# Optimization experiments

Hardware: AMD Instinct MI355X
Metric: run time of the kernel (lower is better)

The kernel has to match this reference:

```python
import jax, jax.numpy as jnp
import numpy as np

DIM = 768
D_STATE = 16
D_INNER = 2 * DIM  # expand=2


def setup_inputs() -> dict:
    key = jax.random.key(0)
    k_x, k_in, k_conv, k_out = jax.random.split(key, 4)
    B, L = 1, 4096
    x = jax.random.normal(k_x, (B, L, DIM), dtype=jnp.float32)
    # torch Linear weight layout: [out_features, in_features]
    W_in = jax.random.normal(k_in, (3 * D_INNER + 2 * D_STATE, DIM), dtype=jnp.float32) * 0.02
    # depthwise conv1d kernel: [out_ch=d_inner, in_ch/groups=1, k=3]
    W_conv = jax.random.normal(k_conv, (D_INNER, 1, 3), dtype=jnp.float32) * 0.1
    W_out = jax.random.normal(k_out, (DIM, D_INNER), dtype=jnp.float32) * 0.02
    A_log = jnp.log(jnp.tile(jnp.arange(1, D_STATE + 1, dtype=jnp.float32), (D_INNER, 1)))
    D = jnp.ones((D_INNER,), dtype=jnp.float32)
    return {"x": x, "W_in": W_in, "W_conv": W_conv, "W_out": W_out, "A_log": A_log, "D": D}


def reference(x, W_in, W_conv, W_out, A_log, D):
    d_inner = W_conv.shape[0]
    d_state = A_log.shape[1]
    Bsz = x.shape[0]

    xz = x @ W_in.T  # [B, L, 3*d_inner + 2*d_state]
    x_inner, z, B_ssm, C_ssm, delta = jnp.split(
        xz, [d_inner, 2 * d_inner, 2 * d_inner + d_state, 2 * d_inner + 2 * d_state], axis=-1
    )

    # depthwise conv over sequence: [B, d_inner, L]
    xc = jax.lax.conv_general_dilated(
        x_inner.transpose(0, 2, 1), W_conv,
        window_strides=(1,), padding=[(1, 1)], feature_group_count=d_inner,
    ).transpose(0, 2, 1)  # back to [B, L, d_inner]
    xc = jax.nn.silu(xc)

    A = -jnp.exp(A_log)  # [d_inner, d_state]
    delta = jax.nn.softplus(delta)  # [B, L, d_inner]
    dA = jnp.exp(jnp.einsum('bld,dn->bldn', delta, A))           # [B, L, d_inner, d_state]
    dBx = jnp.einsum('bld,bln,bld->bldn', delta, B_ssm, xc)      # delta_B * x fused

    def step(h, inp):
        da_t, dbx_t, c_t = inp  # [B,d,n], [B,d,n], [B,n]
        h = da_t * h + dbx_t
        y_t = jnp.einsum('bdn,bn->bd', h, c_t)
        return h, y_t

    h0 = jnp.zeros((Bsz, d_inner, d_state), dtype=x.dtype)
    _, ys = jax.lax.scan(
        step, h0,
        (dA.transpose(1, 0, 2, 3), dBx.transpose(1, 0, 2, 3), C_ssm.transpose(1, 0, 2)),
    )  # ys: [L, B, d_inner]

    y = ys.transpose(1, 0, 2) + xc * D  # skip connection
    y = y * jax.nn.silu(z)
    return y @ W_out.T  # [B, L, dim]
```

## Files before the change

kernel.cpp:

```cpp
#include <hip/hip_runtime.h>
#include <hip/hip_bf16.h>
#include <math.h>

#define LSEQ   4096
#define DIM    768
#define DINNER 1536
#define DSTATE 16
#define NCOLS  4640
#define NCH    256
#define CLEN   16
#define NPAD   4736
#define DXW    1568

typedef _Float16 f16;
typedef __attribute__((ext_vector_type(2))) _Float16 f16x2;
typedef __attribute__((ext_vector_type(4))) _Float16 f16x4;
typedef __attribute__((ext_vector_type(8))) _Float16 f16x8;
typedef __attribute__((ext_vector_type(4))) float f32x4;

__device__ __forceinline__ void gld_lds16(void* lds_dst, const void* gsrc) {
    __builtin_amdgcn_global_load_lds(
        (__attribute__((address_space(1))) void*)(gsrc),
        (__attribute__((address_space(3))) void*)(lds_dst), 16, 0, 0);
}

#define G1K    768
#define G1_NT  12
#define G1_BM  256
#define G1_BN  128
#define G1_RT  384
#define G1_LDSE (G1_RT * 64)

__global__ __launch_bounds__(512) void gemm1_pipe(const f16* __restrict__ A,
                                                  const f16* __restrict__ B,
                                                  float* __restrict__ C,
                                                  f16* __restrict__ Xb,
                                                  f16* __restrict__ Zb) {
    __shared__ __align__(16) f16 S[3 * G1_LDSE];

    const int P   = gridDim.x >> 3;
    const int idx = (blockIdx.x & 7) * P + (blockIdx.x >> 3);
    const int sm  = idx / 296;
    const int rem = idx - sm * 296;
    const int m0  = (sm * 8 + (rem & 7)) * G1_BM;
    const int n0  = (rem >> 3) * G1_BN;

    const int tid  = threadIdx.x;
    const int w    = tid >> 6;
    const int lane = tid & 63;
    const int wr   = w >> 1;
    const int wc   = w & 1;
    const int m    = lane & 15;
    const int q    = lane >> 4;
    const int rl8  = lane >> 3;
    const int bsel = lane & 7;

    const f16* gb[6];
#pragma unroll
    for (int s = 0; s < 6; ++s) {
        const int rl  = (w + 8 * s) * 8 + rl8;
        const int blk = bsel ^ (rl & 7);
        gb[s] = (rl < G1_BM) ? A + (size_t)(m0 + rl) * G1K + blk * 8
                             : B + (size_t)(n0 + rl - G1_BM) * G1K + blk * 8;
    }

    f32x4 acc[4][4];
#pragma unroll
    for (int i = 0; i < 4; i++)
#pragma unroll
        for (int j = 0; j < 4; j++) acc[i][j] = (f32x4){0.f, 0.f, 0.f, 0.f};

    auto stg2 = [&](int kt, int s0) {
        f16* dst = S + (kt % 3) * G1_LDSE;
#pragma unroll
        for (int s = s0; s < s0 + 2; ++s)
            gld_lds16(dst + (w + 8 * s) * 512, gb[s] + kt * 64);
    };
    auto stg6 = [&](int kt) {
        f16* dst = S + (kt % 3) * G1_LDSE;
#pragma unroll
        for (int s = 0; s < 6; ++s)
            gld_lds16(dst + (w + 8 * s) * 512, gb[s] + kt * 64);
    };

    stg6(0);
    stg6(1);

#pragma unroll
    for (int kt = 0; kt < G1_NT; ++kt) {
        if (kt < G1_NT - 1) asm volatile("s_waitcnt vmcnt(6)" ::: "memory");
        else                asm volatile("s_waitcnt vmcnt(0)" ::: "memory");
        __builtin_amdgcn_s_barrier();
        const f16* As = S + (kt % 3) * G1_LDSE;
        const f16* Bs = As + G1_BM * 64;
        const bool pf = (kt + 2 < G1_NT);

        f16x8 af0[2][2], af2[2][2], bh0[2][2], bh2[2][2];

#pragma unroll
        for (int kk = 0; kk < 2; ++kk) {
            const int fo = (((q + 4 * kk) ^ (m & 7)) << 3);
#pragma unroll
            for (int i = 0; i < 2; ++i) {
                af0[kk][i] = *(const f16x8*)&As[(wr * 64 + i * 16 + m) * 64 + fo];
                bh0[kk][i] = *(const f16x8*)&Bs[(wc * 64 + i * 16 + m) * 64 + fo];
            }
        }
        if (pf) stg2(kt + 2, 0);
        __builtin_amdgcn_s_barrier();
        asm volatile("s_waitcnt lgkmcnt(0)" ::: "memory");
        __builtin_amdgcn_sched_barrier(0);
        __builtin_amdgcn_s_setprio(1);
#pragma unroll
        for (int kk = 0; kk < 2; ++kk)
#pragma unroll
            for (int i = 0; i < 2; ++i)
#pragma unroll
                for (int j = 0; j < 2; ++j)
                    acc[i][j] = __builtin_amdgcn_mfma_f32_16x16x32_f16(
                        af0[kk][i], bh0[kk][j], acc[i][j], 0, 0, 0);
        __builtin_amdgcn_s_setprio(0);

#pragma unroll
        for (int kk = 0; kk < 2; ++kk) {
            const int fo = (((q + 4 * kk) ^ (m & 7)) << 3);
#pragma unroll
            for (int j = 0; j < 2; ++j)
                bh2[kk][j] = *(const f16x8*)&Bs[(wc * 64 + (j + 2) * 16 + m) * 64 + fo];
        }
        if (pf) stg2(kt + 2, 2);
        __builtin_amdgcn_s_barrier();
        asm volatile("s_waitcnt lgkmcnt(0)" ::: "memory");
        __builtin_amdgcn_sched_barrier(0);
        __builtin_amdgcn_s_setprio(1);
#pragma unroll
        for (int kk = 0; kk < 2; ++kk)
#pragma unroll
            for (int i = 0; i < 2; ++i)
#pragma unroll
                for (int j = 0; j < 2; ++j)
                    acc[i][j + 2] = __builtin_amdgcn_mfma_f32_16x16x32_f16(
                        af0[kk][i], bh2[kk][j], acc[i][j + 2], 0, 0, 0);
        __builtin_amdgcn_s_setprio(0);

#pragma unroll
        for (int kk = 0; kk < 2; ++kk) {
            const int fo = (((q + 4 * kk) ^ (m & 7)) << 3);
#pragma unroll
            for (int i = 0; i < 2; ++i)
                af2[kk][i] = *(const f16x8*)&As[(wr * 64 + (i + 2) * 16 + m) * 64 + fo];
        }
        if (pf) stg2(kt + 2, 4);
        __builtin_amdgcn_s_barrier();
        asm volatile("s_waitcnt lgkmcnt(0)" ::: "memory");
        __builtin_amdgcn_sched_barrier(0);
        __builtin_amdgcn_s_setprio(1);
#pragma unroll
        for (int kk = 0; kk < 2; ++kk)
#pragma unroll
            for (int i = 0; i < 2; ++i)
#pragma unroll
                for (int j = 0; j < 2; ++j)
                    acc[i + 2][j] = __builtin_amdgcn_mfma_f32_16x16x32_f16(
                        af2[kk][i], bh0[kk][j], acc[i + 2][j], 0, 0, 0);
        __builtin_amdgcn_s_setprio(0);

        __builtin_amdgcn_s_setprio(1);
#pragma unroll
        for (int kk = 0; kk < 2; ++kk)
#pragma unroll
            for (int i = 0; i < 2; ++i)
#pragma unroll
                for (int j = 0; j < 2; ++j)
                    acc[i + 2][j + 2] = __builtin_amdgcn_mfma_f32_16x16x32_f16(
                        af2[kk][i], bh2[kk][j], acc[i + 2][j + 2], 0, 0, 0);
        __builtin_amdgcn_s_setprio(0);
    }

    if (n0 < DINNER) {
#pragma unroll
        for (int i = 0; i < 4; i++)
#pragma unroll
            for (int j = 0; j < 4; j++) {
                const int col  = n0 + wc * 64 + j * 16 + m;
                const int rowb = m0 + wr * 64 + i * 16 + q * 4;
#pragma unroll
                for (int r = 0; r < 4; r++)
                    Xb[(size_t)(rowb + r) * DINNER + col] = (f16)acc[i][j][r];
            }
        return;
    }
    if (n0 < 2 * DINNER) {
#pragma unroll
        for (int i = 0; i < 4; i++)
#pragma unroll
            for (int j = 0; j < 4; j++) {
                const int col  = n0 - DINNER + wc * 64 + j * 16 + m;
                const int rowb = m0 + wr * 64 + i * 16 + q * 4;
#pragma unroll
                for (int r = 0; r < 4; r++)
                    Zb[(size_t)(rowb + r) * DINNER + col] = (f16)acc[i][j][r];
            }
        return;
    }
#pragma unroll
    for (int i = 0; i < 4; i++)
#pragma unroll
        for (int j = 0; j < 4; j++) {
            const int col = n0 - 2 * DINNER + wc * 64 + j * 16 + m;
            if (col >= DXW) continue;
            const int rowb = m0 + wr * 64 + i * 16 + q * 4;
#pragma unroll
            for (int r = 0; r < 4; r++)
                C[(size_t)(rowb + r) * DXW + col] = acc[i][j][r];
        }
}

#define G2K    1536
#define G2_NT  24
#define G2_LDSE (128 * 64)

__global__ __launch_bounds__(256) void gemm2_pipe(const f16* __restrict__ A,
                                                  const f16* __restrict__ B,
                                                  float* __restrict__ C) {
    __shared__ __align__(16) f16 S[3 * G2_LDSE];

    const int P   = gridDim.x >> 3;
    const int idx = (blockIdx.x & 7) * P + (blockIdx.x >> 3);
    const int m0  = (idx / 12) * 64;
    const int n0  = (idx % 12) * 64;

    const int tid  = threadIdx.x;
    const int w    = tid >> 6;
    const int lane = tid & 63;
    const int wr   = w >> 1;
    const int wc   = w & 1;
    const int m    = lane & 15;
    const int q    = lane >> 4;
    const int rl8  = lane >> 3;
    const int bsel = lane & 7;

    const f16* gb[4];
#pragma unroll
    for (int s = 0; s < 4; ++s) {
        const int rl  = (w + 4 * s) * 8 + rl8;
        const int blk = bsel ^ (rl & 7);
        gb[s] = (rl < 64) ? A + (size_t)(m0 + rl) * G2K + blk * 8
                          : B + (size_t)(n0 + rl - 64) * G2K + blk * 8;
    }

    f32x4 acc[2][2];
#pragma unroll
    for (int i = 0; i < 2; i++)
#pragma unroll
        for (int j = 0; j < 2; j++) acc[i][j] = (f32x4){0.f, 0.f, 0.f, 0.f};

    auto stg = [&](int kt) {
        f16* dst = S + (kt % 3) * G2_LDSE;
#pragma unroll
        for (int s = 0; s < 4; ++s)
            gld_lds16(dst + (w + 4 * s) * 512, gb[s] + kt * 64);
    };

    stg(0);
    stg(1);

#pragma unroll
    for (int kt = 0; kt < G2_NT; ++kt) {
        if (kt < G2_NT - 1) asm volatile("s_waitcnt vmcnt(4)" ::: "memory");
        else                asm volatile("s_waitcnt vmcnt(0)" ::: "memory");
        __builtin_amdgcn_s_barrier();
        if (kt + 2 < G2_NT) stg(kt + 2);

        const f16* As = S + (kt % 3) * G2_LDSE;
        const f16* Bs = As + 64 * 64;

        f16x8 af[2][2], bh[2][2];
#pragma unroll
        for (int kk = 0; kk < 2; ++kk) {
            const int fo = (((q + 4 * kk) ^ (m & 7)) << 3);
#pragma unroll
            for (int i = 0; i < 2; ++i) {
                af[kk][i] = *(const f16x8*)&As[(wr * 32 + i * 16 + m) * 64 + fo];
                bh[kk][i] = *(const f16x8*)&Bs[(wc * 32 + i * 16 + m) * 64 + fo];
            }
        }
        asm volatile("s_waitcnt lgkmcnt(0)" ::: "memory");
        __builtin_amdgcn_sched_barrier(0);
        __builtin_amdgcn_s_setprio(1);
#pragma unroll
        for (int kk = 0; kk < 2; ++kk)
#pragma unroll
            for (int i = 0; i < 2; ++i)
#pragma unroll
                for (int j = 0; j < 2; ++j)
                    acc[i][j] = __builtin_amdgcn_mfma_f32_16x16x32_f16(
                        af[kk][i], bh[kk][j], acc[i][j], 0, 0, 0);
        __builtin_amdgcn_s_setprio(0);
    }

#pragma unroll
    for (int i = 0; i < 2; i++)
#pragma unroll
        for (int j = 0; j < 2; j++) {
            const int col  = n0 + wc * 32 + j * 16 + m;
            const int rowb = m0 + wr * 32 + i * 16 + q * 4;
#pragma unroll
            for (int r = 0; r < 4; r++)
                C[(size_t)(rowb + r) * DIM + col] = acc[i][j][r];
        }
}

#define E0 (LSEQ * DIM)
#define E1 (E0 + NPAD * DIM)
#define E2 (E1 + DIM * DINNER)

__global__ __launch_bounds__(256) void cvt_all(const float* __restrict__ x,
                                               const float* __restrict__ Wi,
                                               const float* __restrict__ Wo,
                                               f16* __restrict__ Ax,
                                               f16* __restrict__ Bw,
                                               f16* __restrict__ Bo) {
    int i = (blockIdx.x * 256 + threadIdx.x) * 4;
    if (i < E0) {
        float4 v = *(const float4*)(x + i);
        f16x4 o = {(f16)v.x, (f16)v.y, (f16)v.z, (f16)v.w};
        *(f16x4*)(Ax + i) = o;
    } else if (i < E1) {
        int e = i - E0;
        int n = e / DIM;
        if (n < NCOLS) {
            float4 v = *(const float4*)(Wi + e);
            f16x4 o = {(f16)v.x, (f16)v.y, (f16)v.z, (f16)v.w};
            *(f16x4*)(Bw + e) = o;
        } else {
            f16x4 o = {(f16)0.f, (f16)0.f, (f16)0.f, (f16)0.f};
            *(f16x4*)(Bw + e) = o;
        }
    } else if (i < E2) {
        int e = i - E1;
        float4 v = *(const float4*)(Wo + e);
        f16x4 o = {(f16)v.x, (f16)v.y, (f16)v.z, (f16)v.w};
        *(f16x4*)(Bo + e) = o;
    }
}

__global__ __launch_bounds__(256, 3) void scan1_kernel(const float* __restrict__ Dxz,
                                                       const f16* __restrict__ Xb,
                                                       const float* __restrict__ Wc,
                                                       const float* __restrict__ A_log,
                                                       float* __restrict__ Sb,
                                                       float* __restrict__ hend) {
    __shared__ __align__(16) f16   Xs[18 * 512];
    __shared__ __align__(16) float Ds[16 * 512];
    __shared__ float Bs[CLEN * DSTATE];
    const int tid  = threadIdx.x;
    const int w4   = tid >> 6;
    const int lane = tid & 63;
    const int ch0  = blockIdx.x * 512;
    const int d0   = ch0 + 2 * tid;
    const int c    = blockIdx.y;
    const int l0   = c * CLEN;

    for (int r = w4; r < 18; r += 4) {
        const int gr = l0 - 1 + r;
        if (gr >= 0 && gr < LSEQ)
            gld_lds16(Xs + r * 512, Xb + (size_t)gr * DINNER + ch0 + lane * 8);
    }
    for (int i = w4; i < 32; i += 4) {
        const int t = i >> 1, hh = i & 1;
        gld_lds16(Ds + t * 512 + hh * 256,
                  Dxz + (size_t)(l0 + t) * DXW + 32 + ch0 + hh * 256 + lane * 4);
    }
    for (int i = tid; i < CLEN * DSTATE; i += 256)
        Bs[i] = Dxz[(size_t)(l0 + (i >> 4)) * DXW + (i & 15)];

    float Ar0[DSTATE], Ar1[DSTATE];
#pragma unroll
    for (int n = 0; n < DSTATE; n++) {
        Ar0[n] = -__expf(A_log[d0 * DSTATE + n]);
        Ar1[n] = -__expf(A_log[(d0 + 1) * DSTATE + n]);
    }
    const float w00 = Wc[d0 * 3 + 0], w01 = Wc[d0 * 3 + 1], w02 = Wc[d0 * 3 + 2];
    const float w10 = Wc[d0 * 3 + 3], w11 = Wc[d0 * 3 + 4], w12 = Wc[d0 * 3 + 5];

    asm volatile("s_waitcnt vmcnt(0)" ::: "memory");
    if (l0 == 0)
        *(f16x2*)&Xs[2 * tid] = (f16x2){(f16)0.f, (f16)0.f};
    if (c == NCH - 1)
        *(f16x2*)&Xs[17 * 512 + 2 * tid] = (f16x2){(f16)0.f, (f16)0.f};
    __syncthreads();

    auto ldx = [&](int r) -> float2 {
        f16x2 v = *(const f16x2*)&Xs[r * 512 + 2 * tid];
        return make_float2((float)v.x, (float)v.y);
    };

    float h0[DSTATE], h1[DSTATE];
#pragma unroll
    for (int n = 0; n < DSTATE; n++) { h0[n] = 0.f; h1[n] = 0.f; }
    float S0 = 0.f, S1 = 0.f;

    float2 xm = ldx(0);
    float2 x0 = ldx(1);
    for (int t = 0; t < CLEN; t++) {
        float2 xp = ldx(t + 2);
        float2 dr = *(const float2*)&Ds[t * 512 + 2 * tid];
        float v0  = xm.x * w00 + x0.x * w01 + xp.x * w02;
        float v1  = xm.y * w10 + x0.y * w11 + xp.y * w12;
        float xc0 = __fdividef(v0, 1.f + __expf(-v0));
        float xc1 = __fdividef(v1, 1.f + __expf(-v1));
        float dt0 = (dr.x > 20.f) ? dr.x : __logf(1.f + __expf(dr.x));
        float dt1 = (dr.y > 20.f) ? dr.y : __logf(1.f + __expf(dr.y));
        float u0 = dt0 * xc0, u1 = dt1 * xc1;
        S0 += dt0; S1 += dt1;
#pragma unroll
        for (int n = 0; n < DSTATE; n++) {
            float b = Bs[t * DSTATE + n];
            h0[n] = __expf(dt0 * Ar0[n]) * h0[n] + u0 * b;
            h1[n] = __expf(dt1 * Ar1[n]) * h1[n] + u1 * b;
        }
        xm = x0; x0 = xp;
    }
    *(float2*)&Sb[(size_t)c * DINNER + d0] = make_float2(S0, S1);
#pragma unroll
    for (int n = 0; n < DSTATE; n++)
        *(float2*)&hend[((size_t)c * DSTATE + n) * DINNER + d0] = make_float2(h0[n], h1[n]);
}

__global__ __launch_bounds__(256) void scan2_kernel(const float* __restrict__ Sb,
                                                    const float* __restrict__ A_log,
                                                    const float* __restrict__ hend,
                                                    float* __restrict__ hinit) {
    __shared__ float As_[16][17];
    __shared__ float Es_[16][17];
    __shared__ float Hs_[16][17];
    const int tid = threadIdx.x;
    const int el  = tid & 15;
    const int grp = tid >> 4;
    const int g   = blockIdx.x * 16 + el;
    const int n   = g / DINNER;
    const int d   = g - n * DINNER;
    const float Ar = -__expf(A_log[d * DSTATE + n]);
    const size_t S = (size_t)DSTATE * DINNER;

    float sv[16], ev[16];
#pragma unroll
    for (int k = 0; k < 16; ++k) {
        const int c = grp * 16 + k;
        sv[k] = Sb[(size_t)c * DINNER + d];
        ev[k] = hend[(size_t)c * S + g];
    }
    float av[16];
    float A = 1.f, E = 0.f;
#pragma unroll
    for (int k = 0; k < 16; ++k) {
        av[k] = __expf(sv[k] * Ar);
        E = av[k] * E + ev[k];
        A = av[k] * A;
    }
    As_[grp][el] = A;
    Es_[grp][el] = E;
    __syncthreads();
    if (tid < 16) {
        float h = 0.f;
#pragma unroll
        for (int gq = 0; gq < 16; ++gq) {
            Hs_[gq][tid] = h;
            h = As_[gq][tid] * h + Es_[gq][tid];
        }
    }
    __syncthreads();
    float h = Hs_[grp][el];
#pragma unroll
    for (int k = 0; k < 16; ++k) {
        const int c = grp * 16 + k;
        hinit[(size_t)c * S + g] = h;
        h = av[k] * h + ev[k];
    }
}

__global__ __launch_bounds__(256, 3) void scan3_kernel(const float* __restrict__ Dxz,
                                                       const f16* __restrict__ Xb,
                                                       const f16* __restrict__ Zb,
                                                       const float* __restrict__ Wc,
                                                       const float* __restrict__ A_log,
                                                       const float* __restrict__ hinit,
                                                       const float* __restrict__ Dp,
                                                       f16* __restrict__ Ay) {
    __shared__ __align__(16) f16   Xs[18 * 512];
    __shared__ __align__(16) float Ds[16 * 512];
    __shared__ float Bs[CLEN * DSTATE];
    __shared__ float Cs[CLEN * DSTATE];
    const int tid  = threadIdx.x;
    const int w4   = tid >> 6;
    const int lane = tid & 63;
    const int ch0  = blockIdx.x * 512;
    const int d0   = ch0 + 2 * tid;
    const int c    = blockIdx.y;
    const int l0   = c * CLEN;

    for (int r = w4; r < 18; r += 4) {
        const int gr = l0 - 1 + r;
        if (gr >= 0 && gr < LSEQ)
            gld_lds16(Xs + r * 512, Xb + (size_t)gr * DINNER + ch0 + lane * 8);
    }
    for (int i = w4; i < 32; i += 4) {
        const int t = i >> 1, hh = i & 1;
        gld_lds16(Ds + t * 512 + hh * 256,
                  Dxz + (size_t)(l0 + t) * DXW + 32 + ch0 + hh * 256 + lane * 4);
    }
    for (int i = tid; i < CLEN * DSTATE; i += 256) {
        size_t roff = (size_t)(l0 + (i >> 4)) * DXW;
        Bs[i] = Dxz[roff + (i & 15)];
        Cs[i] = Dxz[roff + 16 + (i & 15)];
    }

    float Ar0[DSTATE], Ar1[DSTATE];
#pragma unroll
    for (int n = 0; n < DSTATE; n++) {
        Ar0[n] = -__expf(A_log[d0 * DSTATE + n]);
        Ar1[n] = -__expf(A_log[(d0 + 1) * DSTATE + n]);
    }
    float h0[DSTATE], h1[DSTATE];
#pragma unroll
    for (int n = 0; n < DSTATE; n++) {
        float2 hv = *(const float2*)&hinit[((size_t)c * DSTATE + n) * DINNER + d0];
        h0[n] = hv.x; h1[n] = hv.y;
    }
    const float Dv0 = Dp[d0], Dv1 = Dp[d0 + 1];
    const float w00 = Wc[d0 * 3 + 0], w01 = Wc[d0 * 3 + 1], w02 = Wc[d0 * 3 + 2];
    const float w10 = Wc[d0 * 3 + 3], w11 = Wc[d0 * 3 + 4], w12 = Wc[d0 * 3 + 5];

    auto ldz2 = [&](int l) -> float2 {
        f16x2 v = *(const f16x2*)&Zb[(size_t)l * DINNER + d0];
        return make_float2((float)v.x, (float)v.y);
    };
    float2 ld_z = ldz2(l0);

    asm volatile("s_waitcnt vmcnt(0)" ::: "memory");
    if (l0 == 0)
        *(f16x2*)&Xs[2 * tid] = (f16x2){(f16)0.f, (f16)0.f};
    if (c == NCH - 1)
        *(f16x2*)&Xs[17 * 512 + 2 * tid] = (f16x2){(f16)0.f, (f16)0.f};
    __syncthreads();

    auto ldx = [&](int r) -> float2 {
        f16x2 v = *(const f16x2*)&Xs[r * 512 + 2 * tid];
        return make_float2((float)v.x, (float)v.y);
    };

    float2 xm = ldx(0);
    float2 x0 = ldx(1);
    for (int t = 0; t < CLEN; t++) {
        const int l = l0 + t;
        float2 xp = ldx(t + 2);
        float2 dr = *(const float2*)&Ds[t * 512 + 2 * tid];
        float2 zv = ld_z;
        if (t + 1 < CLEN) ld_z = ldz2(l + 1);
        float v0  = xm.x * w00 + x0.x * w01 + xp.x * w02;
        float v1  = xm.y * w10 + x0.y * w11 + xp.y * w12;
        float xc0 = __fdividef(v0, 1.f + __expf(-v0));
        float xc1 = __fdividef(v1, 1.f + __expf(-v1));
        float dt0 = (dr.x > 20.f) ? dr.x : __logf(1.f + __expf(dr.x));
        float dt1 = (dr.y > 20.f) ? dr.y : __logf(1.f + __expf(dr.y));
        float u0 = dt0 * xc0, u1 = dt1 * xc1;
        float y0 = 0.f, y1 = 0.f;
#pragma unroll
        for (int n = 0; n < DSTATE; n++) {
            float b  = Bs[t * DSTATE + n];
            float cc = Cs[t * DSTATE + n];
            h0[n] = __expf(dt0 * Ar0[n]) * h0[n] + u0 * b;
            h1[n] = __expf(dt1 * Ar1[n]) * h1[n] + u1 * b;
            y0 += h0[n] * cc;
            y1 += h1[n] * cc;
        }
        float sz0 = __fdividef(zv.x, 1.f + __expf(-zv.x));
        float sz1 = __fdividef(zv.y, 1.f + __expf(-zv.y));
        f16x2 o = {(f16)((y0 + xc0 * Dv0) * sz0), (f16)((y1 + xc1 * Dv1) * sz1)};
        *(f16x2*)&Ay[(size_t)l * DINNER + d0] = o;
        xm = x0; x0 = xp;
    }
}

extern "C" void kernel_launch(void* const* d_in, const int* in_sizes, int n_in,
                              void* d_out, int out_size, void* d_ws, size_t ws_size,
                              hipStream_t stream) {
    const float* x     = (const float*)d_in[0];
    const float* W_in  = (const float*)d_in[1];
    const float* W_conv= (const float*)d_in[2];
    const float* W_out = (const float*)d_in[3];
    const float* A_log = (const float*)d_in[4];
    const float* Dp    = (const float*)d_in[5];
    float* out = (float*)d_out;

    float* ws  = (float*)d_ws;
    float* Dxz = ws;
    float* hi  = Dxz + (size_t)LSEQ * DXW;
    float* he  = hi + (size_t)NCH * DSTATE * DINNER;
    float* Sb  = he + (size_t)NCH * DSTATE * DINNER;
    f16* Ax = (f16*)(Sb + (size_t)NCH * DINNER);
    f16* Ay = Ax + (size_t)LSEQ * DIM;
    f16* Bw = Ay + (size_t)LSEQ * DINNER;
    f16* Bo = Bw + (size_t)NPAD * DIM;
    f16* Zb = Bo + (size_t)DIM * DINNER;
    f16* Xb = Zb + (size_t)LSEQ * DINNER;

    cvt_all<<<E2 / 1024, 256, 0, stream>>>(x, W_in, W_out, Ax, Bw, Bo);

    gemm1_pipe<<<592, 512, 0, stream>>>(Ax, Bw, Dxz, Xb, Zb);

    scan1_kernel<<<dim3(DINNER / 512, NCH), 256, 0, stream>>>(
        Dxz, Xb, W_conv, A_log, Sb, he);
    scan2_kernel<<<(DINNER * DSTATE) / 16, 256, 0, stream>>>(Sb, A_log, he, hi);
    scan3_kernel<<<dim3(DINNER / 512, NCH), 256, 0, stream>>>(
        Dxz, Xb, Zb, W_conv, A_log, hi, Dp, Ay);

    gemm2_pipe<<<768, 256, 0, stream>>>(Ay, Bo, out);
}
```

Baseline: 234.3 us.

## Compute zero-init local scan outputs in pass one and correct with decayed carry in pass three

The first chunked-scan pass now also computes each chunk's local output (zero initial state) together with the prefix-summed delta, writing both to workspace. The last pass no longer reruns the recurrence. It adds the carried-in state's contribution through exp(cumulative delta * A) times C, and the carry pass updates the chunk states in place. This removes the duplicated recurrence from pass three but adds extra global writes and reads of the per-timestep local output and cumulative delta, plus 16 extra exponentials per step in pass three.

```diff
diff --git a/kernel.cpp b/kernel.cpp
--- a/kernel.cpp
+++ b/kernel.cpp
@@ -345,15 +345,17 @@
     }
 }
 
-__global__ __launch_bounds__(256, 3) void scan1_kernel(const float* __restrict__ Dxz,
+__global__ __launch_bounds__(256, 3) void scan1_kernel(float* __restrict__ Dxz,
                                                        const f16* __restrict__ Xb,
                                                        const float* __restrict__ Wc,
                                                        const float* __restrict__ A_log,
                                                        float* __restrict__ Sb,
-                                                       float* __restrict__ hend) {
+                                                       float* __restrict__ hend,
+                                                       float* __restrict__ Y1) {
     __shared__ __align__(16) f16   Xs[18 * 512];
     __shared__ __align__(16) float Ds[16 * 512];
     __shared__ float Bs[CLEN * DSTATE];
+    __shared__ float Cs[CLEN * DSTATE];
     const int tid  = threadIdx.x;
     const int w4   = tid >> 6;
     const int lane = tid & 63;
@@ -372,8 +374,11 @@
         gld_lds16(Ds + t * 512 + hh * 256,
                   Dxz + (size_t)(l0 + t) * DXW + 32 + ch0 + hh * 256 + lane * 4);
     }
-    for (int i = tid; i < CLEN * DSTATE; i += 256)
-        Bs[i] = Dxz[(size_t)(l0 + (i >> 4)) * DXW + (i & 15)];
+    for (int i = tid; i < CLEN * DSTATE; i += 256) {
+        size_t roff = (size_t)(l0 + (i >> 4)) * DXW;
+        Bs[i] = Dxz[roff + (i & 15)];
+        Cs[i] = Dxz[roff + 16 + (i & 15)];
+    }
 
     float Ar0[DSTATE], Ar1[DSTATE];
 #pragma unroll
@@ -404,6 +409,7 @@
     float2 xm = ldx(0);
     float2 x0 = ldx(1);
     for (int t = 0; t < CLEN; t++) {
+        const int l = l0 + t;
         float2 xp = ldx(t + 2);
         float2 dr = *(const float2*)&Ds[t * 512 + 2 * tid];
         float v0  = xm.x * w00 + x0.x * w01 + xp.x * w02;
@@ -414,12 +420,18 @@
         float dt1 = (dr.y > 20.f) ? dr.y : __logf(1.f + __expf(dr.y));
         float u0 = dt0 * xc0, u1 = dt1 * xc1;
         S0 += dt0; S1 += dt1;
+        float y0 = 0.f, y1a = 0.f;
 #pragma unroll
         for (int n = 0; n < DSTATE; n++) {
-            float b = Bs[t * DSTATE + n];
+            float b  = Bs[t * DSTATE + n];
+            float cc = Cs[t * DSTATE + n];
             h0[n] = __expf(dt0 * Ar0[n]) * h0[n] + u0 * b;
             h1[n] = __expf(dt1 * Ar1[n]) * h1[n] + u1 * b;
-        }
+            y0  += h0[n] * cc;
+            y1a += h1[n] * cc;
+        }
+        *(float2*)&Dxz[(size_t)l * DXW + 32 + d0] = make_float2(S0, S1);
+        *(float2*)&Y1[(size_t)l * DINNER + d0]    = make_float2(y0, y1a);
         xm = x0; x0 = xp;
     }
     *(float2*)&Sb[(size_t)c * DINNER + d0] = make_float2(S0, S1);
@@ -430,8 +442,7 @@
 
 __global__ __launch_bounds__(256) void scan2_kernel(const float* __restrict__ Sb,
                                                     const float* __restrict__ A_log,
-                                                    const float* __restrict__ hend,
-                                                    float* __restrict__ hinit) {
+                                                    float* __restrict__ h_io) {
     __shared__ float As_[16][17];
     __shared__ float Es_[16][17];
     __shared__ float Hs_[16][17];
@@ -449,7 +460,7 @@
     for (int k = 0; k < 16; ++k) {
         const int c = grp * 16 + k;
         sv[k] = Sb[(size_t)c * DINNER + d];
-        ev[k] = hend[(size_t)c * S + g];
+        ev[k] = h_io[(size_t)c * S + g];
     }
     float av[16];
     float A = 1.f, E = 0.f;
@@ -475,46 +486,27 @@
 #pragma unroll
     for (int k = 0; k < 16; ++k) {
         const int c = grp * 16 + k;
-        hinit[(size_t)c * S + g] = h;
+        h_io[(size_t)c * S + g] = h;
         h = av[k] * h + ev[k];
     }
 }
 
-__global__ __launch_bounds__(256, 3) void scan3_kernel(const float* __restrict__ Dxz,
-                                                       const f16* __restrict__ Xb,
-                                                       const f16* __restrict__ Zb,
-                                                       const float* __restrict__ Wc,
-                                                       const float* __restrict__ A_log,
-                                                       const float* __restrict__ hinit,
-                                                       const float* __restrict__ Dp,
-                                                       f16* __restrict__ Ay) {
-    __shared__ __align__(16) f16   Xs[18 * 512];
-    __shared__ __align__(16) float Ds[16 * 512];
-    __shared__ float Bs[CLEN * DSTATE];
+__global__ __launch_bounds__(256) void scan3_kernel(const float* __restrict__ Dxz,
+                                                    const f16* __restrict__ Xb,
+                                                    const f16* __restrict__ Zb,
+                                                    const float* __restrict__ Wc,
+                                                    const float* __restrict__ A_log,
+                                                    const float* __restrict__ hin,
+                                                    const float* __restrict__ Y1,
+                                                    const float* __restrict__ Dp,
+                                                    f16* __restrict__ Ay) {
     __shared__ float Cs[CLEN * DSTATE];
-    const int tid  = threadIdx.x;
-    const int w4   = tid >> 6;
-    const int lane = tid & 63;
-    const int ch0  = blockIdx.x * 512;
-    const int d0   = ch0 + 2 * tid;
-    const int c    = blockIdx.y;
-    const int l0   = c * CLEN;
-
-    for (int r = w4; r < 18; r += 4) {
-        const int gr = l0 - 1 + r;
-        if (gr >= 0 && gr < LSEQ)
-            gld_lds16(Xs + r * 512, Xb + (size_t)gr * DINNER + ch0 + lane * 8);
-    }
-    for (int i = w4; i < 32; i += 4) {
-        const int t = i >> 1, hh = i & 1;
-        gld_lds16(Ds + t * 512 + hh * 256,
-                  Dxz + (size_t)(l0 + t) * DXW + 32 + ch0 + hh * 256 + lane * 4);
-    }
-    for (int i = tid; i < CLEN * DSTATE; i += 256) {
-        size_t roff = (size_t)(l0 + (i >> 4)) * DXW;
-        Bs[i] = Dxz[roff + (i & 15)];
-        Cs[i] = Dxz[roff + 16 + (i & 15)];
-    }
+    const int tid = threadIdx.x;
+    const int d0  = (blockIdx.x * 256 + tid) * 2;
+    const int c   = blockIdx.y;
+    const int l0  = c * CLEN;
+    for (int i = tid; i < CLEN * DSTATE; i += 256)
+        Cs[i] = Dxz[(size_t)(l0 + (i >> 4)) * DXW + 16 + (i & 15)];
 
     float Ar0[DSTATE], Ar1[DSTATE];
 #pragma unroll
@@ -522,62 +514,49 @@
         Ar0[n] = -__expf(A_log[d0 * DSTATE + n]);
         Ar1[n] = -__expf(A_log[(d0 + 1) * DSTATE + n]);
     }
-    float h0[DSTATE], h1[DSTATE];
+    float hin0[DSTATE], hin1[DSTATE];
 #pragma unroll
     for (int n = 0; n < DSTATE; n++) {
-        float2 hv = *(const float2*)&hinit[((size_t)c * DSTATE + n) * DINNER + d0];
-        h0[n] = hv.x; h1[n] = hv.y;
+        float2 hv = *(const float2*)&hin[((size_t)c * DSTATE + n) * DINNER + d0];
+        hin0[n] = hv.x; hin1[n] = hv.y;
     }
     const float Dv0 = Dp[d0], Dv1 = Dp[d0 + 1];
     const float w00 = Wc[d0 * 3 + 0], w01 = Wc[d0 * 3 + 1], w02 = Wc[d0 * 3 + 2];
     const float w10 = Wc[d0 * 3 + 3], w11 = Wc[d0 * 3 + 4], w12 = Wc[d0 * 3 + 5];
 
+    auto ldx2 = [&](int l) -> float2 {
+        f16x2 v = *(const f16x2*)&Xb[(size_t)l * DINNER + d0];
+        return make_float2((float)v.x, (float)v.y);
+    };
     auto ldz2 = [&](int l) -> float2 {
         f16x2 v = *(const f16x2*)&Zb[(size_t)l * DINNER + d0];
         return make_float2((float)v.x, (float)v.y);
     };
-    float2 ld_z = ldz2(l0);
-
-    asm volatile("s_waitcnt vmcnt(0)" ::: "memory");
-    if (l0 == 0)
-        *(f16x2*)&Xs[2 * tid] = (f16x2){(f16)0.f, (f16)0.f};
-    if (c == NCH - 1)
-        *(f16x2*)&Xs[17 * 512 + 2 * tid] = (f16x2){(f16)0.f, (f16)0.f};
+    float2 xm = (l0 > 0) ? ldx2(l0 - 1) : make_float2(0.f, 0.f);
+    float2 x0 = ldx2(l0);
     __syncthreads();
 
-    auto ldx = [&](int r) -> float2 {
-        f16x2 v = *(const f16x2*)&Xs[r * 512 + 2 * tid];
-        return make_float2((float)v.x, (float)v.y);
-    };
-
-    float2 xm = ldx(0);
-    float2 x0 = ldx(1);
+#pragma unroll 4
     for (int t = 0; t < CLEN; t++) {
         const int l = l0 + t;
-        float2 xp = ldx(t + 2);
-        float2 dr = *(const float2*)&Ds[t * 512 + 2 * tid];
-        float2 zv = ld_z;
-        if (t + 1 < CLEN) ld_z = ldz2(l + 1);
+        float2 xp = (l + 1 < LSEQ) ? ldx2(l + 1) : make_float2(0.f, 0.f);
+        float2 zv = ldz2(l);
+        float2 sc = *(const float2*)&Dxz[(size_t)l * DXW + 32 + d0];
+        float2 yv = *(const float2*)&Y1[(size_t)l * DINNER + d0];
         float v0  = xm.x * w00 + x0.x * w01 + xp.x * w02;
         float v1  = xm.y * w10 + x0.y * w11 + xp.y * w12;
         float xc0 = __fdividef(v0, 1.f + __expf(-v0));
         float xc1 = __fdividef(v1, 1.f + __expf(-v1));
-        float dt0 = (dr.x > 20.f) ? dr.x : __logf(1.f + __expf(dr.x));
-        float dt1 = (dr.y > 20.f) ? dr.y : __logf(1.f + __expf(dr.y));
-        float u0 = dt0 * xc0, u1 = dt1 * xc1;
-        float y0 = 0.f, y1 = 0.f;
+        float y0 = yv.x, y1a = yv.y;
 #pragma unroll
         for (int n = 0; n < DSTATE; n++) {
-            float b  = Bs[t * DSTATE + n];
             float cc = Cs[t * DSTATE + n];
-            h0[n] = __expf(dt0 * Ar0[n]) * h0[n] + u0 * b;
-            h1[n] = __expf(dt1 * Ar1[n]) * h1[n] + u1 * b;
-            y0 += h0[n] * cc;
-            y1 += h1[n] * cc;
+            y0  += cc * __expf(sc.x * Ar0[n]) * hin0[n];
+            y1a += cc * __expf(sc.y * Ar1[n]) * hin1[n];
         }
         float sz0 = __fdividef(zv.x, 1.f + __expf(-zv.x));
         float sz1 = __fdividef(zv.y, 1.f + __expf(-zv.y));
-        f16x2 o = {(f16)((y0 + xc0 * Dv0) * sz0), (f16)((y1 + xc1 * Dv1) * sz1)};
+        f16x2 o = {(f16)((y0 + xc0 * Dv0) * sz0), (f16)((y1a + xc1 * Dv1) * sz1)};
         *(f16x2*)&Ay[(size_t)l * DINNER + d0] = o;
         xm = x0; x0 = xp;
     }
@@ -596,8 +575,8 @@
 
     float* ws  = (float*)d_ws;
     float* Dxz = ws;
-    float* hi  = Dxz + (size_t)LSEQ * DXW;
-    float* he  = hi + (size_t)NCH * DSTATE * DINNER;
+    float* Y1  = Dxz + (size_t)LSEQ * DXW;
+    float* he  = Y1 + (size_t)LSEQ * DINNER;
     float* Sb  = he + (size_t)NCH * DSTATE * DINNER;
     f16* Ax = (f16*)(Sb + (size_t)NCH * DINNER);
     f16* Ay = Ax + (size_t)LSEQ * DIM;
@@ -611,10 +590,10 @@
     gemm1_pipe<<<592, 512, 0, stream>>>(Ax, Bw, Dxz, Xb, Zb);
 
     scan1_kernel<<<dim3(DINNER / 512, NCH), 256, 0, stream>>>(
-        Dxz, Xb, W_conv, A_log, Sb, he);
-    scan2_kernel<<<(DINNER * DSTATE) / 16, 256, 0, stream>>>(Sb, A_log, he, hi);
+        Dxz, Xb, W_conv, A_log, Sb, he, Y1);
+    scan2_kernel<<<(DINNER * DSTATE) / 16, 256, 0, stream>>>(Sb, A_log, he);
     scan3_kernel<<<dim3(DINNER / 512, NCH), 256, 0, stream>>>(
-        Dxz, Xb, Zb, W_conv, A_log, hi, Dp, Ay);
+        Dxz, Xb, Zb, W_conv, A_log, he, Y1, Dp, Ay);
 
     gemm2_pipe<<<768, 256, 0, stream>>>(Ay, Bo, out);
 }
```

Measured after the change: 238.7 us. No clear change (+1.9%).
